# Optimization experiments

Hardware: AMD Instinct MI355X
Metric: run time of the kernel (lower is better)

The kernel has to match this reference:

```python
import jax, jax.numpy as jnp
import numpy as np

EMBED_DIM = 1024
NUM_HEADS = 16
HEAD_DIM = EMBED_DIM // NUM_HEADS


def setup_inputs() -> dict:
    key = jax.random.key(0)
    ks = jax.random.split(key, 9)
    s = 1.0 / np.sqrt(EMBED_DIM)
    x = jax.random.normal(ks[0], (2, 2048, EMBED_DIM), dtype=jnp.float32)
    Wq = jax.random.uniform(ks[1], (EMBED_DIM, EMBED_DIM), jnp.float32, -s, s)
    bq = jax.random.uniform(ks[2], (EMBED_DIM,), jnp.float32, -s, s)
    Wk = jax.random.uniform(ks[3], (EMBED_DIM, EMBED_DIM), jnp.float32, -s, s)
    bk = jax.random.uniform(ks[4], (EMBED_DIM,), jnp.float32, -s, s)
    Wv = jax.random.uniform(ks[5], (EMBED_DIM, EMBED_DIM), jnp.float32, -s, s)
    bv = jax.random.uniform(ks[6], (EMBED_DIM,), jnp.float32, -s, s)
    Wo = jax.random.uniform(ks[7], (EMBED_DIM, EMBED_DIM), jnp.float32, -s, s)
    bo = jax.random.uniform(ks[8], (EMBED_DIM,), jnp.float32, -s, s)
    return {"x": x, "Wq": Wq, "bq": bq, "Wk": Wk, "bk": bk,
            "Wv": Wv, "bv": bv, "Wo": Wo, "bo": bo}


def reference(x, Wq, bq, Wk, bk, Wv, bv, Wo, bo):
    B, N, C = x.shape
    H, D = NUM_HEADS, HEAD_DIM
    # nn.Linear: y = x @ W.T + b; here W stored as [in, out] so y = x @ W + b
    def split_heads(y):
        return y.reshape(B, N, H, D).transpose(0, 2, 1, 3)  # [B,H,N,D]
    q = split_heads(x @ Wq + bq)
    k = split_heads(x @ Wk + bk)
    v = split_heads(x @ Wv + bv)
    scores = jnp.einsum('bhnd,bhmd->bhnm', q, k) / jnp.sqrt(jnp.float32(D)).astype(x.dtype)
    attn = jax.nn.softmax(scores, axis=-1)
    ctx = jnp.einsum('bhnm,bhmd->bhnd', attn, v)
    ctx = ctx.transpose(0, 2, 1, 3).reshape(B, N, C)
    return ctx @ Wo + bo
```

## Files before the change

### kernel.cpp

```cpp
#include <hip/hip_runtime.h>
#include <hip/hip_bf16.h>
#include <stdint.h>
#include <stddef.h>

using bf16 = __hip_bfloat16;
using bf16x8 = __attribute__((ext_vector_type(8))) short;
using f32x4  = __attribute__((ext_vector_type(4))) float;
using f32x16 = __attribute__((ext_vector_type(16))) float;
typedef unsigned int u32x2 __attribute__((ext_vector_type(2)));
typedef unsigned int u32x4 __attribute__((ext_vector_type(4)));

#define MFMA16(a, b, c) __builtin_amdgcn_mfma_f32_16x16x32_bf16((a), (b), (c), 0, 0, 0)
#define MFMA32(a, b, c) __builtin_amdgcn_mfma_f32_32x32x16_bf16((a), (b), (c), 0, 0, 0)

#define GLD16(g, l)                                                            \
  __builtin_amdgcn_global_load_lds(                                            \
      (const __attribute__((address_space(1))) void*)(g),                      \
      (__attribute__((address_space(3))) void*)(l), 16, 0, 0)

__device__ __forceinline__ float exp2_fast(float x) {
#if __has_builtin(__builtin_amdgcn_exp2f)
  return __builtin_amdgcn_exp2f(x);
#else
  return __expf(x * 0.69314718056f);
#endif
}

__device__ __forceinline__ float fmax3(float a, float b, float c) {
  return fmaxf(fmaxf(a, b), c);
}

__device__ __forceinline__ unsigned int cvtpk_bf16(float lo, float hi) {
  unsigned int r;
  asm("v_cvt_pk_bf16_f32 %0, %1, %2" : "=v"(r) : "v"(lo), "v"(hi));
  return r;
}

__device__ __forceinline__ void permswap(unsigned int& a, unsigned int& b, int hi) {
#if __has_builtin(__builtin_amdgcn_permlane32_swap)
  u32x2 r = __builtin_amdgcn_permlane32_swap(a, b, false, false);
  a = r.x;
  b = r.y;
#else
  unsigned int sa = __shfl_xor((unsigned int)a, 32, 64);
  unsigned int sb = __shfl_xor((unsigned int)b, 32, 64);
  unsigned int an = hi ? sb : a;
  unsigned int bn = hi ? b : sa;
  a = an; b = bn;
#endif
}


__global__ void convert_x(const float* __restrict__ x, bf16* __restrict__ out) {
  const int i = blockIdx.x * 256 + threadIdx.x;
  const float4 v = ((const float4*)x)[i];
  __hip_bfloat162* o2 = (__hip_bfloat162*)(out + (size_t)i * 4);
  o2[0] = __float22bfloat162_rn(make_float2(v.x, v.y));
  o2[1] = __float22bfloat162_rn(make_float2(v.z, v.w));
}

__global__ void convert_w(const float* __restrict__ W0, const float* __restrict__ W1,
                          const float* __restrict__ W2, const float* __restrict__ W3,
                          bf16* __restrict__ Wt) {
  __shared__ float t[32][33];
  const int bx = blockIdx.x;
  const int mat = bx >> 10;
  const float* W = (mat == 0) ? W0 : (mat == 1) ? W1 : (mat == 2) ? W2 : W3;
  const int rem = bx & 1023;
  const int k0 = (rem >> 5) * 32, n0 = (rem & 31) * 32;
  const int c = threadIdx.x & 31, r0 = (threadIdx.x >> 5) * 4;
#pragma unroll
  for (int i = 0; i < 4; ++i) {
    const int r = r0 + i;
    t[r][c] = W[(size_t)(k0 + r) * 1024 + n0 + c];
  }
  __syncthreads();
  bf16* dst = Wt + (size_t)mat * 1024 * 1024;
#pragma unroll
  for (int i = 0; i < 4; ++i) {
    const int rn = r0 + i;
    dst[(size_t)(n0 + rn) * 1024 + k0 + c] = __float2bfloat16(t[c][rn]);
  }
}

__global__ void concat_bias(const float* __restrict__ bq, const float* __restrict__ bk,
                            const float* __restrict__ bv, const float* __restrict__ bo,
                            float* __restrict__ dst) {
  const int i = blockIdx.x * 256 + threadIdx.x;
  const float* src = (i < 1024) ? bq : (i < 2048) ? bk : (i < 3072) ? bv : bo;
  dst[i] = src[i & 1023];
}

__global__ __launch_bounds__(512, 2)
void gemm_qkv(const bf16* __restrict__ A, const bf16* __restrict__ Bt,
              const float* __restrict__ bias,
              bf16* __restrict__ Qb, bf16* __restrict__ Kb, bf16* __restrict__ Vt) {
  __shared__ bf16 Abuf[2][2][128 * 64];
  __shared__ bf16 Bbuf[2][2][128 * 64];
  const int tid = threadIdx.x;
  const int lane = tid & 63, w = tid >> 6;
  const int wr = w >> 2, wc = w & 3;
  const int lrow = lane & 15, lgk = lane >> 4;

  const int bid = blockIdx.x;
  const int xcd = bid & 7, i6 = bid >> 3;
  const int xr = xcd >> 1, xc = xcd & 1;
  const int bm = (xr * 4 + (i6 & 3)) * 256;
  const int bn = (xc * 6 + (i6 >> 2)) * 256;

  f32x4 acc[8][4] = {};

  auto stageA = [&](int b, int hh, int kt) {
#pragma unroll
    for (int u = 0; u < 2; ++u) {
      const int c = u * 512 + tid;
      const int r = c >> 3, j = c & 7;
      GLD16(A + (size_t)(bm + hh * 128 + r) * 1024 + kt * 64 + ((j ^ (r & 7)) * 8),
            &Abuf[b][hh][c * 8]);
    }
  };
  auto stageB = [&](int b, int hh, int kt) {
#pragma unroll
    for (int u = 0; u < 2; ++u) {
      const int c = u * 512 + tid;
      const int r = c >> 3, j = c & 7;
      GLD16(Bt + (size_t)(bn + hh * 128 + r) * 1024 + kt * 64 + ((j ^ (r & 7)) * 8),
            &Bbuf[b][hh][c * 8]);
    }
  };

  bf16x8 a_[8];
  bf16x8 b0_[4], b1_[4];

  auto readA = [&](int b, int mg, bf16x8 (&dst)[8]) {
#pragma unroll
    for (int mf = 0; mf < 4; ++mf)
#pragma unroll
      for (int kk = 0; kk < 2; ++kk) {
        const int r = (mg * 4 + mf) * 16 + lrow;
        const int s = (kk * 4 + lgk) ^ (lrow & 7);
        dst[mf * 2 + kk] = *(const bf16x8*)(&Abuf[b][wr][(r * 8 + s) * 8]);
      }
  };
  auto readB = [&](int b, int ng, bf16x8 (&dst)[4]) {
#pragma unroll
    for (int nf = 0; nf < 2; ++nf)
#pragma unroll
      for (int kk = 0; kk < 2; ++kk) {
        const int r = (wc & 1) * 64 + (ng * 2 + nf) * 16 + lrow;
        const int s = (kk * 4 + lgk) ^ (lrow & 7);
        dst[nf * 2 + kk] = *(const bf16x8*)(&Bbuf[b][wc >> 1][(r * 8 + s) * 8]);
      }
  };

  stageA(0, 0, 0);
  stageA(0, 1, 0);
  stageB(0, 0, 0);
  stageB(0, 1, 0);

  for (int t = 0; t < 16; ++t) {
    const int b = t & 1, nb = b ^ 1;
    if (t < 15) {
      stageA(nb, 0, t + 1);
      asm volatile("s_waitcnt vmcnt(2)" ::: "memory");
    } else {
      asm volatile("s_waitcnt vmcnt(0)" ::: "memory");
    }
    __builtin_amdgcn_s_barrier();
    readA(b, 0, a_);
    readB(b, 0, b0_);
    asm volatile("s_waitcnt lgkmcnt(0)" ::: "memory");
    __builtin_amdgcn_sched_barrier(0);
    __builtin_amdgcn_s_setprio(1);
#pragma unroll
    for (int mf = 0; mf < 4; ++mf)
#pragma unroll
      for (int nf = 0; nf < 2; ++nf)
#pragma unroll
        for (int kk = 0; kk < 2; ++kk)
          acc[mf][nf] = MFMA16(a_[mf * 2 + kk], b0_[nf * 2 + kk], acc[mf][nf]);
    __builtin_amdgcn_s_setprio(0);
    __builtin_amdgcn_s_barrier();
    readB(b, 1, b1_);
    if (t < 15) stageA(nb, 1, t + 1);
    __builtin_amdgcn_s_barrier();
    asm volatile("s_waitcnt lgkmcnt(0)" ::: "memory");
    __builtin_amdgcn_sched_barrier(0);
    __builtin_amdgcn_s_setprio(1);
#pragma unroll
    for (int mf = 0; mf < 4; ++mf)
#pragma unroll
      for (int nf = 0; nf < 2; ++nf)
#pragma unroll
        for (int kk = 0; kk < 2; ++kk)
          acc[mf][2 + nf] = MFMA16(a_[mf * 2 + kk], b1_[nf * 2 + kk], acc[mf][2 + nf]);
    __builtin_amdgcn_s_setprio(0);
    __builtin_amdgcn_s_barrier();
    readA(b, 1, a_);
    if (t < 15) stageB(nb, 0, t + 1);
    __builtin_amdgcn_s_barrier();
    asm volatile("s_waitcnt lgkmcnt(0)" ::: "memory");
    __builtin_amdgcn_sched_barrier(0);
    __builtin_amdgcn_s_setprio(1);
#pragma unroll
    for (int mf = 0; mf < 4; ++mf)
#pragma unroll
      for (int nf = 0; nf < 2; ++nf)
#pragma unroll
        for (int kk = 0; kk < 2; ++kk)
          acc[4 + mf][2 + nf] =
              MFMA16(a_[mf * 2 + kk], b1_[nf * 2 + kk], acc[4 + mf][2 + nf]);
    __builtin_amdgcn_s_setprio(0);
    __builtin_amdgcn_s_barrier();
    if (t < 15) stageB(nb, 1, t + 1);
    __builtin_amdgcn_s_setprio(1);
#pragma unroll
    for (int mf = 0; mf < 4; ++mf)
#pragma unroll
      for (int nf = 0; nf < 2; ++nf)
#pragma unroll
        for (int kk = 0; kk < 2; ++kk)
          acc[4 + mf][nf] = MFMA16(a_[mf * 2 + kk], b0_[nf * 2 + kk], acc[4 + mf][nf]);
    __builtin_amdgcn_s_setprio(0);
    __builtin_amdgcn_s_barrier();
  }

  const int which = bn >> 10;
#pragma unroll
  for (int mf = 0; mf < 8; ++mf) {
#pragma unroll
    for (int nf = 0; nf < 4; ++nf) {
      const int col = bn + wc * 64 + nf * 16 + lrow;
      const float bv_ = bias[col];
      const int row0 = bm + wr * 128 + mf * 16 + lgk * 4;
      const int hd = col & 1023;
      const int h = hd >> 6, d = hd & 63;
      const int bb = row0 >> 11, t0 = row0 & 2047;
      const int bh = bb * 16 + h;
      if (which == 2) {
        uint2 pk;
        pk.x = cvtpk_bf16(acc[mf][nf][0] + bv_, acc[mf][nf][1] + bv_);
        pk.y = cvtpk_bf16(acc[mf][nf][2] + bv_, acc[mf][nf][3] + bv_);
        *(uint2*)(Vt + ((size_t)bh * 64 + d) * 2048 + t0) = pk;
      } else if (which == 0) {
#pragma unroll
        for (int j = 0; j < 4; ++j)
          Qb[((size_t)bh * 2048 + t0 + j) * 64 + d] =
              __float2bfloat16((acc[mf][nf][j] + bv_) * 0.18033688f);
      } else {
#pragma unroll
        for (int j = 0; j < 4; ++j)
          Kb[((size_t)bh * 2048 + t0 + j) * 64 + d] =
              __float2bfloat16(acc[mf][nf][j] + bv_);
      }
    }
  }
}

__global__ __launch_bounds__(256)
void gemm_o(const bf16* __restrict__ A, const bf16* __restrict__ Bt,
            const float* __restrict__ bias, float* __restrict__ Of, int K) {
  __shared__ bf16 As[3][128 * 32];
  __shared__ bf16 Bs[3][64 * 32];
  const int tid = threadIdx.x;
  const int lane = tid & 63, w = tid >> 6;
  const int wr = w >> 1, wc = w & 1;
  const int lrow = lane & 15, lgk = lane >> 4;
  const int bm = blockIdx.y * 128, bn = blockIdx.x * 64;
  f32x4 acc[4][2] = {};
  const bf16* Ab = A + (size_t)bm * K;
  const bf16* Bb = Bt + (size_t)bn * K;
  const int e0 = tid, e1 = 256 + tid;
  const int NT = K >> 5;

  auto stage = [&](int s, int k0) {
    GLD16(Ab + (size_t)(e0 >> 2) * K + k0 + (e0 & 3) * 8, &As[s][e0 * 8]);
    GLD16(Ab + (size_t)(e1 >> 2) * K + k0 + (e1 & 3) * 8, &As[s][e1 * 8]);
    GLD16(Bb + (size_t)(e0 >> 2) * K + k0 + (e0 & 3) * 8, &Bs[s][e0 * 8]);
  };

  stage(0, 0);
  stage(1, 32);
  int cur = 0, nxt = 2;
  for (int t = 0; t < NT; ++t) {
    if (t < NT - 1)
      asm volatile("s_waitcnt vmcnt(3)" ::: "memory");
    else
      asm volatile("s_waitcnt vmcnt(0)" ::: "memory");
    __builtin_amdgcn_s_barrier();
    if (t + 2 < NT) {
      stage(nxt, (t + 2) << 5);
      nxt = (nxt == 2) ? 0 : nxt + 1;
    }
    bf16x8 af[4], bfr[2];
#pragma unroll
    for (int m = 0; m < 4; ++m)
      af[m] = *(const bf16x8*)(&As[cur][(wr * 64 + m * 16 + lrow) * 32 + lgk * 8]);
#pragma unroll
    for (int n = 0; n < 2; ++n)
      bfr[n] = *(const bf16x8*)(&Bs[cur][(wc * 32 + n * 16 + lrow) * 32 + lgk * 8]);
#pragma unroll
    for (int m = 0; m < 4; ++m)
#pragma unroll
      for (int n = 0; n < 2; ++n)
        acc[m][n] = MFMA16(af[m], bfr[n], acc[m][n]);
    cur = (cur == 2) ? 0 : cur + 1;
  }

#pragma unroll
  for (int m = 0; m < 4; ++m) {
#pragma unroll
    for (int n = 0; n < 2; ++n) {
      const int col = bn + wc * 32 + n * 16 + lrow;
      const float bv_ = bias[col];
      const int row0 = bm + wr * 64 + m * 16 + lgk * 4;
#pragma unroll
      for (int j = 0; j < 4; ++j)
        Of[(size_t)(row0 + j) * 1024 + col] = acc[m][n][j] + bv_;
    }
  }
}

__global__ __launch_bounds__(256, 2)
void attn_kernel(const bf16* __restrict__ Q, const bf16* __restrict__ Kb,
                 const bf16* __restrict__ Vt, bf16* __restrict__ ctx) {
  __shared__ bf16 Kl[2][64 * 64];
  __shared__ bf16 Vl[2][64 * 64];

  const int tid = threadIdx.x, lane = tid & 63, w = tid >> 6;
  const int lo5 = lane & 31, hi = lane >> 5;

  const int bid = blockIdx.x;
  const int xcd = bid & 7, idx = bid >> 3;
  const int bh = (xcd << 2) | (idx >> 4);
  const int qt = idx & 15;
  const int q0 = qt * 128 + w * 32;

  const bf16* Qbh = Q + (size_t)bh * 2048 * 64;
  const bf16* Kbh = Kb + (size_t)bh * 2048 * 64;
  const bf16* Vbh = Vt + (size_t)bh * 64 * 2048;

  bf16x8 qf[4];
#pragma unroll
  for (int f = 0; f < 4; ++f)
    qf[f] = *(const bf16x8*)(Qbh + (size_t)(q0 + lo5) * 64 + f * 16 + hi * 8);

  f32x16 o0 = {}, o1 = {};
  float m2 = -1e30f;
  float lsum = 0.f;

  auto stage = [&](int buf, int kv) {
#pragma unroll
    for (int i = 0; i < 2; ++i) {
      const int c = (w * 2 + i) * 64 + lane;
      const int r = c >> 3, j = c & 7;
      const int js = (j ^ (r & 7)) * 8;
      GLD16(Kbh + (size_t)(kv + r) * 64 + js, &Kl[buf][c * 8]);
      GLD16(Vbh + (size_t)r * 2048 + kv + js, &Vl[buf][c * 8]);
    }
  };

  bf16x8 pa[4];

  auto softmax_pa = [&](f32x16& s0, f32x16& s1) {
    float r1[11];
#pragma unroll
    for (int i = 0; i < 5; ++i)
      r1[i] = fmax3(s0[3 * i], s0[3 * i + 1], s0[3 * i + 2]);
    r1[5] = fmax3(s0[15], s1[0], s1[1]);
#pragma unroll
    for (int i = 0; i < 4; ++i)
      r1[6 + i] = fmax3(s1[2 + 3 * i], s1[3 + 3 * i], s1[4 + 3 * i]);
    r1[10] = fmaxf(s1[14], s1[15]);
    float r2[4];
#pragma unroll
    for (int i = 0; i < 3; ++i) r2[i] = fmax3(r1[3 * i], r1[3 * i + 1], r1[3 * i + 2]);
    r2[3] = fmaxf(r1[9], r1[10]);
    const float pm = fmaxf(fmax3(r2[0], r2[1], r2[2]), r2[3]);
    if (!__all(pm <= m2 + 11.5416f)) {
      const float mx = fmaxf(pm, __shfl_xor(pm, 32, 64));
      const float mn = fmaxf(m2, mx);
      const float corr = exp2_fast(m2 - mn);
      m2 = mn;
      lsum *= corr;
#pragma unroll
      for (int j = 0; j < 16; ++j) { o0[j] *= corr; o1[j] *= corr; }
    }
#pragma unroll
    for (int j = 0; j < 16; ++j) s0[j] = exp2_fast(s0[j] - m2);
#pragma unroll
    for (int j = 0; j < 16; ++j) s1[j] = exp2_fast(s1[j] - m2);
    float a8[8];
#pragma unroll
    for (int j = 0; j < 8; ++j) a8[j] = (s0[j] + s0[j + 8]) + (s1[j] + s1[j + 8]);
    float a4[4];
#pragma unroll
    for (int j = 0; j < 4; ++j) a4[j] = a8[j] + a8[j + 4];
    lsum += (a4[0] + a4[1]) + (a4[2] + a4[3]);
#pragma unroll
    for (int ks = 0; ks < 4; ++ks) {
      const f32x16& s = (ks < 2) ? s0 : s1;
      const int b0 = (ks & 1) * 8;
      unsigned int a0 = cvtpk_bf16(s[b0 + 0], s[b0 + 1]);
      unsigned int c0 = cvtpk_bf16(s[b0 + 4], s[b0 + 5]);
      unsigned int a1 = cvtpk_bf16(s[b0 + 2], s[b0 + 3]);
      unsigned int c1 = cvtpk_bf16(s[b0 + 6], s[b0 + 7]);
      permswap(a0, c0, hi);
      permswap(a1, c1, hi);
      u32x4 tt;
      tt.x = a0; tt.y = a1; tt.z = c0; tt.w = c1;
      pa[ks] = __builtin_bit_cast(bf16x8, tt);
    }
  };

  f32x16 sA0, sA1, sB0, sB1;
  bf16x8 vfA[8], vfB[8];

  auto step = [&](int t, f32x16& sC0, f32x16& sC1, bf16x8 (&vfC)[8],
                  f32x16& sP0, f32x16& sP1, bf16x8 (&vfP)[8]) {
    const int cur = t & 1;
    const int kv = t << 6;
    if (t < 31) stage(cur ^ 1, kv + 64);
    if (t < 31)
      asm volatile("s_waitcnt vmcnt(4)" ::: "memory");
    else
      asm volatile("s_waitcnt vmcnt(0)" ::: "memory");
    __builtin_amdgcn_s_barrier();
    bf16x8 kf[8];
#pragma unroll
    for (int kt = 0; kt < 2; ++kt)
#pragma unroll
      for (int f = 0; f < 4; ++f) {
        const int r = kt * 32 + lo5;
        kf[kt * 4 + f] =
            *(const bf16x8*)(&Kl[cur][(r * 8 + (((f << 1) + hi) ^ (r & 7))) * 8]);
      }
#pragma unroll
    for (int dt = 0; dt < 2; ++dt)
#pragma unroll
      for (int ks = 0; ks < 4; ++ks) {
        const int r = dt * 32 + lo5;
        vfC[dt * 4 + ks] =
            *(const bf16x8*)(&Vl[cur][(r * 8 + (((ks << 1) + hi) ^ (r & 7))) * 8]);
      }
    if (t > 0) softmax_pa(sP0, sP1);
    asm volatile("s_waitcnt lgkmcnt(0)" ::: "memory");
    __builtin_amdgcn_sched_barrier(0);
    __builtin_amdgcn_s_barrier();
    __builtin_amdgcn_s_setprio(1);
    sC0 = f32x16{};
    sC1 = f32x16{};
#pragma unroll
    for (int f = 0; f < 4; ++f) sC0 = MFMA32(kf[f], qf[f], sC0);
#pragma unroll
    for (int f = 0; f < 4; ++f) sC1 = MFMA32(kf[4 + f], qf[f], sC1);
    if (t > 0) {
#pragma unroll
      for (int ks = 0; ks < 4; ++ks) {
        o0 = MFMA32(vfP[ks], pa[ks], o0);
        o1 = MFMA32(vfP[4 + ks], pa[ks], o1);
      }
    }
    __builtin_amdgcn_s_setprio(0);
  };

  stage(0, 0);

  step(0, sA0, sA1, vfA, sB0, sB1, vfB);
  for (int tt = 1; tt < 31; tt += 2) {
    step(tt, sB0, sB1, vfB, sA0, sA1, vfA);
    step(tt + 1, sA0, sA1, vfA, sB0, sB1, vfB);
  }
  step(31, sB0, sB1, vfB, sA0, sA1, vfA);

  softmax_pa(sB0, sB1);
#pragma unroll
  for (int ks = 0; ks < 4; ++ks) {
    o0 = MFMA32(vfB[ks], pa[ks], o0);
    o1 = MFMA32(vfB[4 + ks], pa[ks], o1);
  }

  lsum += __shfl_xor(lsum, 32, 64);
  const float inv = 1.f / lsum;
  const int b = bh >> 4, h = bh & 15;
  bf16* crow = ctx + (size_t)(b * 2048 + q0 + lo5) * 1024 + h * 64;
#pragma unroll
  for (int g = 0; g < 4; ++g) {
    uint2 pk0, pk1;
    pk0.x = cvtpk_bf16(o0[4 * g + 0] * inv, o0[4 * g + 1] * inv);
    pk0.y = cvtpk_bf16(o0[4 * g + 2] * inv, o0[4 * g + 3] * inv);
    pk1.x = cvtpk_bf16(o1[4 * g + 0] * inv, o1[4 * g + 1] * inv);
    pk1.y = cvtpk_bf16(o1[4 * g + 2] * inv, o1[4 * g + 3] * inv);
    *(uint2*)(crow + 8 * g + 4 * hi) = pk0;
    *(uint2*)(crow + 32 + 8 * g + 4 * hi) = pk1;
  }
}


extern "C" void kernel_launch(void* const* d_in, const int* in_sizes, int n_in,
                              void* d_out, int out_size, void* d_ws, size_t ws_size,
                              hipStream_t stream) {
  const float* x  = (const float*)d_in[0];
  const float* Wq = (const float*)d_in[1];
  const float* bq = (const float*)d_in[2];
  const float* Wk = (const float*)d_in[3];
  const float* bk = (const float*)d_in[4];
  const float* Wv = (const float*)d_in[5];
  const float* bv = (const float*)d_in[6];
  const float* Wo = (const float*)d_in[7];
  const float* bo = (const float*)d_in[8];
  float* out = (float*)d_out;

  char* ws = (char*)d_ws;
  bf16* xb  = (bf16*)(ws);
  bf16* Wt  = (bf16*)(ws + ((size_t)8 << 20));
  bf16* Qb  = (bf16*)(ws + ((size_t)16 << 20));
  bf16* Kb  = (bf16*)(ws + ((size_t)24 << 20));
  bf16* Vt  = (bf16*)(ws + ((size_t)32 << 20));
  bf16* ctx = (bf16*)(ws + ((size_t)40 << 20));
  float* ba = (float*)(ws + ((size_t)48 << 20));

  convert_x<<<dim3(4096), dim3(256), 0, stream>>>(x, xb);
  convert_w<<<dim3(4096), dim3(256), 0, stream>>>(Wq, Wk, Wv, Wo, Wt);
  concat_bias<<<dim3(16), dim3(256), 0, stream>>>(bq, bk, bv, bo, ba);

  gemm_qkv<<<dim3(192), dim3(512), 0, stream>>>(xb, Wt, ba, Qb, Kb, Vt);

  attn_kernel<<<dim3(512), dim3(256), 0, stream>>>(Qb, Kb, Vt, ctx);

  gemm_o<<<dim3(16, 32), dim3(256), 0, stream>>>(
      ctx, Wt + (size_t)3072 * 1024, ba + 3072, out, 1024);
}
```

Baseline: 123.4 us.

## Retile QKV GEMM to 128x384 blocks with 256 workgroups and deeper A prefetch

The QKV projection GEMM switches from 256x256 tiles on 192 blocks to 128x384 tiles on 256 blocks, so the grid fills all 256 CUs of the MI355X. The pipeline is also restructured: A is prefetched two k-steps ahead, B is staged in three 128-row chunks interleaved with the MFMA phases, and there are fewer barriers per iteration. Because a tile can now straddle the Q/K/V boundary, the Q/K/V target is chosen per column in the epilogue. The trade-off is lower arithmetic intensity per tile and different LDS usage, which may affect occupancy.

```diff
diff --git a/kernel.cpp b/kernel.cpp
--- a/kernel.cpp
+++ b/kernel.cpp
@@ -95,80 +95,79 @@
 void gemm_qkv(const bf16* __restrict__ A, const bf16* __restrict__ Bt,
               const float* __restrict__ bias,
               bf16* __restrict__ Qb, bf16* __restrict__ Kb, bf16* __restrict__ Vt) {
-  __shared__ bf16 Abuf[2][2][128 * 64];
-  __shared__ bf16 Bbuf[2][2][128 * 64];
+  __shared__ bf16 Ab[2][128 * 64];
+  __shared__ bf16 Bb[2][384 * 64];
   const int tid = threadIdx.x;
   const int lane = tid & 63, w = tid >> 6;
   const int wr = w >> 2, wc = w & 3;
   const int lrow = lane & 15, lgk = lane >> 4;
 
   const int bid = blockIdx.x;
-  const int xcd = bid & 7, i6 = bid >> 3;
+  const int xcd = bid & 7, i5 = bid >> 3;
   const int xr = xcd >> 1, xc = xcd & 1;
-  const int bm = (xr * 4 + (i6 & 3)) * 256;
-  const int bn = (xc * 6 + (i6 >> 2)) * 256;
-
-  f32x4 acc[8][4] = {};
-
-  auto stageA = [&](int b, int hh, int kt) {
-#pragma unroll
-    for (int u = 0; u < 2; ++u) {
-      const int c = u * 512 + tid;
+  const int bm = (xr * 8 + (i5 & 7)) * 128;
+  const int bn = (xc * 4 + (i5 >> 3)) * 384;
+
+  f32x4 acc[4][6] = {};
+
+  auto stageA = [&](int b, int kt) {
+#pragma unroll
+    for (int v = 0; v < 2; ++v) {
+      const int c = v * 512 + tid;
       const int r = c >> 3, j = c & 7;
-      GLD16(A + (size_t)(bm + hh * 128 + r) * 1024 + kt * 64 + ((j ^ (r & 7)) * 8),
-            &Abuf[b][hh][c * 8]);
-    }
-  };
-  auto stageB = [&](int b, int hh, int kt) {
-#pragma unroll
-    for (int u = 0; u < 2; ++u) {
-      const int c = u * 512 + tid;
-      const int r = c >> 3, j = c & 7;
-      GLD16(Bt + (size_t)(bn + hh * 128 + r) * 1024 + kt * 64 + ((j ^ (r & 7)) * 8),
-            &Bbuf[b][hh][c * 8]);
-    }
-  };
-
-  bf16x8 a_[8];
-  bf16x8 b0_[4], b1_[4];
-
-  auto readA = [&](int b, int mg, bf16x8 (&dst)[8]) {
+      GLD16(A + (size_t)(bm + r) * 1024 + kt * 64 + ((j ^ (r & 7)) * 8),
+            &Ab[b][c * 8]);
+    }
+  };
+  auto stageB = [&](int b, int kt, int u) {
+#pragma unroll
+    for (int v = 0; v < 2; ++v) {
+      const int cl = v * 512 + tid;
+      const int r = u * 128 + (cl >> 3), j = cl & 7;
+      GLD16(Bt + (size_t)(bn + r) * 1024 + kt * 64 + ((j ^ ((r & 7))) * 8),
+            &Bb[b][(r * 8 + (j)) * 8]);
+    }
+  };
+
+  auto readA = [&](int b, bf16x8 (&dst)[8]) {
 #pragma unroll
     for (int mf = 0; mf < 4; ++mf)
 #pragma unroll
       for (int kk = 0; kk < 2; ++kk) {
-        const int r = (mg * 4 + mf) * 16 + lrow;
-        const int s = (kk * 4 + lgk) ^ (lrow & 7);
-        dst[mf * 2 + kk] = *(const bf16x8*)(&Abuf[b][wr][(r * 8 + s) * 8]);
+        const int r = wr * 64 + mf * 16 + lrow;
+        const int s = (kk * 4 + lgk) ^ (r & 7);
+        dst[mf * 2 + kk] = *(const bf16x8*)(&Ab[b][(r * 8 + s) * 8]);
       }
   };
-  auto readB = [&](int b, int ng, bf16x8 (&dst)[4]) {
+  auto readB2 = [&](int b, int nf0, bf16x8 (&dst)[4]) {
 #pragma unroll
     for (int nf = 0; nf < 2; ++nf)
 #pragma unroll
       for (int kk = 0; kk < 2; ++kk) {
-        const int r = (wc & 1) * 64 + (ng * 2 + nf) * 16 + lrow;
-        const int s = (kk * 4 + lgk) ^ (lrow & 7);
-        dst[nf * 2 + kk] = *(const bf16x8*)(&Bbuf[b][wc >> 1][(r * 8 + s) * 8]);
+        const int r = wc * 96 + (nf0 + nf) * 16 + lrow;
+        const int s = (kk * 4 + lgk) ^ (r & 7);
+        dst[nf * 2 + kk] = *(const bf16x8*)(&Bb[b][(r * 8 + s) * 8]);
       }
   };
 
-  stageA(0, 0, 0);
-  stageA(0, 1, 0);
+  stageA(0, 0);
   stageB(0, 0, 0);
-  stageB(0, 1, 0);
+  stageB(0, 0, 1);
+  stageB(0, 0, 2);
+  stageA(1, 1);
+  asm volatile("s_waitcnt vmcnt(2)" ::: "memory");
+  __builtin_amdgcn_s_barrier();
+
+  bf16x8 a_[8], b01[4], b23[4], b45[4];
 
   for (int t = 0; t < 16; ++t) {
     const int b = t & 1, nb = b ^ 1;
     if (t < 15) {
-      stageA(nb, 0, t + 1);
-      asm volatile("s_waitcnt vmcnt(2)" ::: "memory");
-    } else {
-      asm volatile("s_waitcnt vmcnt(0)" ::: "memory");
-    }
-    __builtin_amdgcn_s_barrier();
-    readA(b, 0, a_);
-    readB(b, 0, b0_);
+      stageB(nb, t + 1, 0);
+      stageB(nb, t + 1, 1);
+    }
+    readA(b, a_);
+    readB2(b, 0, b01);
     asm volatile("s_waitcnt lgkmcnt(0)" ::: "memory");
     __builtin_amdgcn_sched_barrier(0);
     __builtin_amdgcn_s_setprio(1);
@@ -178,12 +177,10 @@
       for (int nf = 0; nf < 2; ++nf)
 #pragma unroll
         for (int kk = 0; kk < 2; ++kk)
-          acc[mf][nf] = MFMA16(a_[mf * 2 + kk], b0_[nf * 2 + kk], acc[mf][nf]);
+          acc[mf][nf] = MFMA16(a_[mf * 2 + kk], b01[nf * 2 + kk], acc[mf][nf]);
     __builtin_amdgcn_s_setprio(0);
-    __builtin_amdgcn_s_barrier();
-    readB(b, 1, b1_);
-    if (t < 15) stageA(nb, 1, t + 1);
-    __builtin_amdgcn_s_barrier();
+    if (t < 15) stageB(nb, t + 1, 2);
+    readB2(b, 2, b23);
     asm volatile("s_waitcnt lgkmcnt(0)" ::: "memory");
     __builtin_amdgcn_sched_barrier(0);
     __builtin_amdgcn_s_setprio(1);
@@ -193,14 +190,13 @@
       for (int nf = 0; nf < 2; ++nf)
 #pragma unroll
         for (int kk = 0; kk < 2; ++kk)
-          acc[mf][2 + nf] = MFMA16(a_[mf * 2 + kk], b1_[nf * 2 + kk], acc[mf][2 + nf]);
+          acc[mf][2 + nf] = MFMA16(a_[mf * 2 + kk], b23[nf * 2 + kk], acc[mf][2 + nf]);
     __builtin_amdgcn_s_setprio(0);
-    __builtin_amdgcn_s_barrier();
-    readA(b, 1, a_);
-    if (t < 15) stageB(nb, 0, t + 1);
-    __builtin_amdgcn_s_barrier();
+    readB2(b, 4, b45);
     asm volatile("s_waitcnt lgkmcnt(0)" ::: "memory");
     __builtin_amdgcn_sched_barrier(0);
+    __builtin_amdgcn_s_barrier();
+    if (t < 14) stageA(b, t + 2);
     __builtin_amdgcn_s_setprio(1);
 #pragma unroll
     for (int mf = 0; mf < 4; ++mf)
@@ -208,31 +204,23 @@
       for (int nf = 0; nf < 2; ++nf)
 #pragma unroll
         for (int kk = 0; kk < 2; ++kk)
-          acc[4 + mf][2 + nf] =
-              MFMA16(a_[mf * 2 + kk], b1_[nf * 2 + kk], acc[4 + mf][2 + nf]);
+          acc[mf][4 + nf] = MFMA16(a_[mf * 2 + kk], b45[nf * 2 + kk], acc[mf][4 + nf]);
     __builtin_amdgcn_s_setprio(0);
+    if (t < 14)
+      asm volatile("s_waitcnt vmcnt(2)" ::: "memory");
+    else
+      asm volatile("s_waitcnt vmcnt(0)" ::: "memory");
     __builtin_amdgcn_s_barrier();
-    if (t < 15) stageB(nb, 1, t + 1);
-    __builtin_amdgcn_s_setprio(1);
-#pragma unroll
-    for (int mf = 0; mf < 4; ++mf)
-#pragma unroll
-      for (int nf = 0; nf < 2; ++nf)
-#pragma unroll
-        for (int kk = 0; kk < 2; ++kk)
-          acc[4 + mf][nf] = MFMA16(a_[mf * 2 + kk], b0_[nf * 2 + kk], acc[4 + mf][nf]);
-    __builtin_amdgcn_s_setprio(0);
-    __builtin_amdgcn_s_barrier();
-  }
-
-  const int which = bn >> 10;
-#pragma unroll
-  for (int mf = 0; mf < 8; ++mf) {
-#pragma unroll
-    for (int nf = 0; nf < 4; ++nf) {
-      const int col = bn + wc * 64 + nf * 16 + lrow;
+  }
+
+#pragma unroll
+  for (int mf = 0; mf < 4; ++mf) {
+#pragma unroll
+    for (int nf = 0; nf < 6; ++nf) {
+      const int col = bn + wc * 96 + nf * 16 + lrow;
       const float bv_ = bias[col];
-      const int row0 = bm + wr * 128 + mf * 16 + lgk * 4;
+      const int row0 = bm + wr * 64 + mf * 16 + lgk * 4;
+      const int which = col >> 10;
       const int hd = col & 1023;
       const int h = hd >> 6, d = hd & 63;
       const int bb = row0 >> 11, t0 = row0 & 2047;
@@ -524,7 +512,7 @@
   convert_w<<<dim3(4096), dim3(256), 0, stream>>>(Wq, Wk, Wv, Wo, Wt);
   concat_bias<<<dim3(16), dim3(256), 0, stream>>>(bq, bk, bv, bo, ba);
 
-  gemm_qkv<<<dim3(192), dim3(512), 0, stream>>>(xb, Wt, ba, Qb, Kb, Vt);
+  gemm_qkv<<<dim3(256), dim3(512), 0, stream>>>(xb, Wt, ba, Qb, Kb, Vt);
 
   attn_kernel<<<dim3(512), dim3(256), 0, stream>>>(Qb, Kb, Vt, ctx);
 
```

Result: no change. 122.1 us (-1.1%).
